# Kernel tuning notes

Hardware: AMD Instinct MI355X
Metric: run time of the kernel (lower is better)

The kernel has to match this reference:

```python
import jax, jax.numpy as jnp
import numpy as np


def _butter1(Wn, highpass):
    """First-order Butterworth digital coefficients (bilinear transform),
    matching scipy.signal.butter(1, Wn, btype). Wn is nyquist-normalized."""
    K = jnp.tan(jnp.pi * Wn / 2.0)
    a1 = (K - 1.0) / (K + 1.0)
    if highpass:
        b0 = 1.0 / (K + 1.0)
        b1 = -b0
    else:
        b0 = K / (K + 1.0)
        b1 = b0
    return b0, b1, a1


def setup_inputs() -> dict:
    key = jax.random.key(0)
    B, T = 128, 262144
    x = jax.random.normal(key, (B, T), dtype=jnp.float32)
    return {
        "x": x,
        "center_freq": jnp.float32(1000.0),  # nn.Parameter
        "bandwidth": jnp.float32(500.0),     # nn.Parameter
        "gain": jnp.float32(1.0),            # nn.Parameter
        "sample_rate": 48000,
    }


def reference(x, center_freq, bandwidth, gain, sample_rate):
    nyq = sample_rate / 2.0
    low_wn = (center_freq - bandwidth / 2.0) / nyq
    high_wn = (center_freq + bandwidth / 2.0) / nyq
    # cascaded 1st-order highpass(low_wn) then lowpass(high_wn) = bandpass
    bh0, bh1, ah1 = _butter1(low_wn, highpass=True)
    bl0, bl1, al1 = _butter1(high_wn, highpass=False)

    xt = x.T  # [T, B] -- scan over time, vectorized over batch
    zeros = jnp.zeros((x.shape[0],), dtype=x.dtype)

    def step(carry, x_t):
        x_prev, y1_prev, y2_prev = carry
        y1 = bh0 * x_t + bh1 * x_prev - ah1 * y1_prev   # highpass stage
        y2 = bl0 * y1 + bl1 * y1_prev - al1 * y2_prev   # lowpass stage
        return (x_t, y1, y2), y2

    _, yt = jax.lax.scan(step, (zeros, zeros, zeros), xt)
    return yt.T * gain  # [B, T]
```

## Files before the change

kernel.cpp:

```cpp
#include <hip/hip_runtime.h>
#include <math.h>

#define B_    128
#define T_    262144
#define L_    16
#define NT_   256
#define WCH_  16
#define OT_   (NT_ * L_)
#define TPR_  (T_ / OT_)
#define NW_   (NT_ / 64)

typedef float f32x4 __attribute__((ext_vector_type(4)));

struct Coef {
    float bh0, bh1;
    float p, q, r;
    float blc0, blc1;
};

__device__ inline void iir_step(const Coef& c, float xt, float& x_prev,
                                float& y1, float& y2) {
    float c1 = fmaf(c.bh0,  xt, c.bh1  * x_prev);
    float cx = fmaf(c.blc0, xt, c.blc1 * x_prev);
    float ny1 = fmaf(c.p, y1, c1);
    float ny2 = fmaf(c.q, y1, fmaf(c.r, y2, cx));
    y1 = ny1; y2 = ny2; x_prev = xt;
}

struct Mat { float p, q, r; };
__device__ inline Mat mat_sq(Mat m) {
    Mat o; o.p = m.p * m.p; o.q = m.q * (m.p + m.r); o.r = m.r * m.r; return o;
}
__device__ inline Mat mat_mul(Mat a, Mat b) {
    Mat o; o.p = a.p * b.p; o.q = fmaf(a.q, b.p, a.r * b.q); o.r = a.r * b.r;
    return o;
}
__device__ inline float2 mat_apply_add(Mat m, float2 v, float2 add) {
    float2 o;
    o.x = fmaf(m.p, v.x, add.x);
    o.y = fmaf(m.q, v.x, fmaf(m.r, v.y, add.y));
    return o;
}

__global__ __launch_bounds__(NT_, 4) void bp_kernel(
        const float* __restrict__ x, float* __restrict__ out,
        const float* __restrict__ cfp, const float* __restrict__ bwp,
        const float* __restrict__ gp, const int* __restrict__ srp) {
    __shared__ float2 wagg[WCH_];
    __shared__ float2 wsagg[NW_];

    const int blk  = blockIdx.x;
    const int row  = blk >> 6;
    const int ti   = blk & (TPR_ - 1);
    const int t    = threadIdx.x;
    const int lane = t & 63;
    const int wav  = t >> 6;
    const long tile_start = (long)row * T_ + (long)ti * OT_;
    const float* xb = x + tile_start;

    const f32x4* xg = (const f32x4*)(xb + t * L_);
    f32x4 v0 = xg[0], v1 = xg[1], v2 = xg[2], v3 = xg[3];
    float xp = (ti != 0 || t != 0) ? xb[t * L_ - 1] : 0.f;
    f32x4 w0 = (f32x4)(0.f), w1 = w0, w2 = w0, w3 = w0;
    float wxp = 0.f;
    if (t < WCH_ && ti != 0) {
        const f32x4* wg = (const f32x4*)(xb - WCH_ * L_ + t * L_);
        w0 = wg[0]; w1 = wg[1]; w2 = wg[2]; w3 = wg[3];
        if (t != 0) wxp = xb[-WCH_ * L_ + t * L_ - 1];
    }

    Coef cf;
    {
        const float PIH = 1.57079632679489661923f;
        float cfv = *cfp, bwv = *bwp;
        float nyq = 0.5f * (float)(*srp);
        float K1 = tanf(PIH * (cfv - 0.5f * bwv) / nyq);
        float K2 = tanf(PIH * (cfv + 0.5f * bwv) / nyq);
        float inv1 = 1.0f / (K1 + 1.0f);
        float ah1 = (K1 - 1.0f) * inv1;
        float inv2 = 1.0f / (K2 + 1.0f);
        float bl0 = K2 * inv2;
        float al1 = (K2 - 1.0f) * inv2;
        cf.bh0 = inv1;
        cf.bh1 = -inv1;
        cf.p = -ah1;
        cf.q = bl0 - bl0 * ah1;
        cf.r = -al1;
        cf.blc0 = bl0 * inv1;
        cf.blc1 = -bl0 * inv1;
    }
    const float gain = *gp;

    Mat A  = { cf.p, cf.q, cf.r };
    Mat AL = A;
    #pragma unroll
    for (int k = 0; k < 4; ++k) AL = mat_sq(AL);
    Mat R = { 1.f, 0.f, 1.f };
    {
        Mat Mp = AL;
        unsigned b = (unsigned)lane;
        #pragma unroll
        for (int k = 0; k < 6; ++k) {
            if (b & 1u) R = mat_mul(Mp, R);
            b >>= 1u;
            if (k < 5) Mp = mat_sq(Mp);
        }
    }

    float xa[L_];
    xa[0]=v0.x; xa[1]=v0.y; xa[2]=v0.z; xa[3]=v0.w;
    xa[4]=v1.x; xa[5]=v1.y; xa[6]=v1.z; xa[7]=v1.w;
    xa[8]=v2.x; xa[9]=v2.y; xa[10]=v2.z; xa[11]=v2.w;
    xa[12]=v3.x; xa[13]=v3.y; xa[14]=v3.z; xa[15]=v3.w;
    float y2l[L_];
    float y1 = 0.f, y2 = 0.f;
    {
        float xprev = xp;
        #pragma unroll
        for (int i = 0; i < L_; ++i) {
            iir_step(cf, xa[i], xprev, y1, y2);
            y2l[i] = y2;
        }
    }

    if (t < WCH_) {
        float wa[L_];
        wa[0]=w0.x; wa[1]=w0.y; wa[2]=w0.z; wa[3]=w0.w;
        wa[4]=w1.x; wa[5]=w1.y; wa[6]=w1.z; wa[7]=w1.w;
        wa[8]=w2.x; wa[9]=w2.y; wa[10]=w2.z; wa[11]=w2.w;
        wa[12]=w3.x; wa[13]=w3.y; wa[14]=w3.z; wa[15]=w3.w;
        float wy1 = 0.f, wy2 = 0.f, wp = wxp;
        #pragma unroll
        for (int i = 0; i < L_; ++i) iir_step(cf, wa[i], wp, wy1, wy2);
        wagg[t] = make_float2(wy1, wy2);
    }

    float2 a = make_float2(y1, y2);
    Mat Pw = AL;
    #pragma unroll
    for (int o = 1; o < 64; o <<= 1) {
        float vx = __shfl_up(a.x, (unsigned)o, 64);
        float vy = __shfl_up(a.y, (unsigned)o, 64);
        if (lane >= o) {
            a.y = fmaf(Pw.q, vx, fmaf(Pw.r, vy, a.y));
            a.x = fmaf(Pw.p, vx, a.x);
        }
        Pw = mat_sq(Pw);
    }
    float2 ex;
    ex.x = __shfl_up(a.x, 1u, 64);
    ex.y = __shfl_up(a.y, 1u, 64);
    if (lane == 0) { ex.x = 0.f; ex.y = 0.f; }
    if (lane == 63) wsagg[wav] = a;
    __syncthreads();

    float2 S = make_float2(0.f, 0.f);
    #pragma unroll
    for (int j = 0; j < WCH_; ++j) S = mat_apply_add(AL, S, wagg[j]);
    #pragma unroll
    for (int u = 0; u < NW_ - 1; ++u)
        if (wav > u) S = mat_apply_add(Pw, S, wsagg[u]);

    float2 E = mat_apply_add(R, S, ex);

    {
        float c1 = E.x, c2 = E.y;
        #pragma unroll
        for (int i = 0; i < L_; ++i) {
            float nc1 = cf.p * c1;
            float nc2 = fmaf(cf.q, c1, cf.r * c2);
            c1 = nc1; c2 = nc2;
            y2l[i] = (y2l[i] + c2) * gain;
        }
    }
    f32x4* og = (f32x4*)(out + tile_start + (long)t * L_);
    f32x4 o0; o0.x = y2l[0];  o0.y = y2l[1];  o0.z = y2l[2];  o0.w = y2l[3];
    f32x4 o1; o1.x = y2l[4];  o1.y = y2l[5];  o1.z = y2l[6];  o1.w = y2l[7];
    f32x4 o2; o2.x = y2l[8];  o2.y = y2l[9];  o2.z = y2l[10]; o2.w = y2l[11];
    f32x4 o3; o3.x = y2l[12]; o3.y = y2l[13]; o3.z = y2l[14]; o3.w = y2l[15];
    __builtin_nontemporal_store(o0, og + 0);
    __builtin_nontemporal_store(o1, og + 1);
    __builtin_nontemporal_store(o2, og + 2);
    __builtin_nontemporal_store(o3, og + 3);
}

extern "C" void kernel_launch(void* const* d_in, const int* in_sizes, int n_in,
                              void* d_out, int out_size, void* d_ws, size_t ws_size,
                              hipStream_t stream) {
    const float* x   = (const float*)d_in[0];
    const float* cfp = (const float*)d_in[1];
    const float* bwp = (const float*)d_in[2];
    const float* gp  = (const float*)d_in[3];
    const int*   srp = (const int*)d_in[4];
    float* out = (float*)d_out;

    dim3 blk(NT_), grd(B_ * TPR_);
    bp_kernel<<<grd, blk, 0, stream>>>(x, out, cfp, bwp, gp, srp);
}
```

Before: 285.3 us.

## Stage outputs through padded LDS for coalesced stores, shuffle prev sample, raise occupancy

Each thread now writes its 16 results into a padded shared-memory buffer, and after a barrier the block stores the tile with fully coalesced float4 writes instead of strided per-thread 64-byte chunks. The scalar global load of the previous sample is replaced by a wave shuffle from the neighbouring lane, with only lane 0 still reading memory. The launch-bounds occupancy hint is raised from 4 to 8 blocks. This adds about 17 KB of LDS per block, an extra barrier and scalar LDS reads, and may force register spilling under the tighter occupancy target.

```diff
diff --git a/kernel.cpp b/kernel.cpp
--- a/kernel.cpp
+++ b/kernel.cpp
@@ -9,6 +9,7 @@
 #define OT_   (NT_ * L_)
 #define TPR_  (T_ / OT_)
 #define NW_   (NT_ / 64)
+#define STR_  (L_ + 1)
 
 typedef float f32x4 __attribute__((ext_vector_type(4)));
 
@@ -42,10 +43,11 @@
     return o;
 }
 
-__global__ __launch_bounds__(NT_, 4) void bp_kernel(
+__global__ __launch_bounds__(NT_, 8) void bp_kernel(
         const float* __restrict__ x, float* __restrict__ out,
         const float* __restrict__ cfp, const float* __restrict__ bwp,
         const float* __restrict__ gp, const int* __restrict__ srp) {
+    __shared__ float  ys[NT_ * STR_];
     __shared__ float2 wagg[WCH_];
     __shared__ float2 wsagg[NW_];
 
@@ -60,14 +62,13 @@
 
     const f32x4* xg = (const f32x4*)(xb + t * L_);
     f32x4 v0 = xg[0], v1 = xg[1], v2 = xg[2], v3 = xg[3];
-    float xp = (ti != 0 || t != 0) ? xb[t * L_ - 1] : 0.f;
     f32x4 w0 = (f32x4)(0.f), w1 = w0, w2 = w0, w3 = w0;
-    float wxp = 0.f;
     if (t < WCH_ && ti != 0) {
         const f32x4* wg = (const f32x4*)(xb - WCH_ * L_ + t * L_);
         w0 = wg[0]; w1 = wg[1]; w2 = wg[2]; w3 = wg[3];
-        if (t != 0) wxp = xb[-WCH_ * L_ + t * L_ - 1];
-    }
+    }
+    float xp = __shfl_up(v3.w, 1u, 64);
+    if (lane == 0) xp = (ti != 0 || t != 0) ? xb[t * L_ - 1] : 0.f;
 
     Coef cf;
     {
@@ -123,13 +124,15 @@
         }
     }
 
+    float wxp = __shfl_up(w3.w, 1u, 64);
     if (t < WCH_) {
         float wa[L_];
         wa[0]=w0.x; wa[1]=w0.y; wa[2]=w0.z; wa[3]=w0.w;
         wa[4]=w1.x; wa[5]=w1.y; wa[6]=w1.z; wa[7]=w1.w;
         wa[8]=w2.x; wa[9]=w2.y; wa[10]=w2.z; wa[11]=w2.w;
         wa[12]=w3.x; wa[13]=w3.y; wa[14]=w3.z; wa[15]=w3.w;
-        float wy1 = 0.f, wy2 = 0.f, wp = wxp;
+        float wy1 = 0.f, wy2 = 0.f;
+        float wp = (t == 0) ? 0.f : wxp;
         #pragma unroll
         for (int i = 0; i < L_; ++i) iir_step(cf, wa[i], wp, wy1, wy2);
         wagg[t] = make_float2(wy1, wy2);
@@ -165,23 +168,26 @@
 
     {
         float c1 = E.x, c2 = E.y;
+        float* cp = ys + t * STR_;
         #pragma unroll
         for (int i = 0; i < L_; ++i) {
             float nc1 = cf.p * c1;
             float nc2 = fmaf(cf.q, c1, cf.r * c2);
             c1 = nc1; c2 = nc2;
-            y2l[i] = (y2l[i] + c2) * gain;
-        }
-    }
-    f32x4* og = (f32x4*)(out + tile_start + (long)t * L_);
-    f32x4 o0; o0.x = y2l[0];  o0.y = y2l[1];  o0.z = y2l[2];  o0.w = y2l[3];
-    f32x4 o1; o1.x = y2l[4];  o1.y = y2l[5];  o1.z = y2l[6];  o1.w = y2l[7];
-    f32x4 o2; o2.x = y2l[8];  o2.y = y2l[9];  o2.z = y2l[10]; o2.w = y2l[11];
-    f32x4 o3; o3.x = y2l[12]; o3.y = y2l[13]; o3.z = y2l[14]; o3.w = y2l[15];
-    __builtin_nontemporal_store(o0, og + 0);
-    __builtin_nontemporal_store(o1, og + 1);
-    __builtin_nontemporal_store(o2, og + 2);
-    __builtin_nontemporal_store(o3, og + 3);
+            cp[i] = (y2l[i] + c2) * gain;
+        }
+    }
+    __syncthreads();
+
+    f32x4* og = (f32x4*)(out + tile_start);
+    #pragma unroll
+    for (int k = 0; k < 4; ++k) {
+        int F = t + NT_ * k;
+        int chunk = F >> 2, pos = 4 * (F & 3);
+        const float* p = ys + chunk * STR_ + pos;
+        f32x4 o; o.x = p[0]; o.y = p[1]; o.z = p[2]; o.w = p[3];
+        __builtin_nontemporal_store(o, og + F);
+    }
 }
 
 extern "C" void kernel_launch(void* const* d_in, const int* in_sizes, int n_in,
```

Measured after the change: 239.1 us. 16.2% less time.
